# Optimization experiments

Measured on AMD Instinct MI355X. Metric: run time of the kernel, lower is better.

## Reference

```python
import jax, jax.numpy as jnp
import numpy as np
import math


def setup_inputs() -> dict:
    key = jax.random.key(0)
    k1, k2, k3 = jax.random.split(key, 3)
    b, h, s, d = 2, 16, 2048, 64
    q = jax.random.normal(k1, (b, h, s, d), dtype=jnp.float32)
    k = jax.random.normal(k2, (b, h, d, s), dtype=jnp.float32)  # pre-transposed as in the torch module
    v = jax.random.normal(k3, (b, h, s, d), dtype=jnp.float32)
    return {"q": q, "k": k, "v": v}


def reference(q, k, v):
    d = q.shape[-1]
    # unnormalized exp-attention, no max subtraction (faithful to source)
    p = jnp.exp(jnp.einsum('bhsd,bhdt->bhst', q, k) / math.sqrt(d))  # [b,h,s,s]
    attn = jnp.einsum('bhst,bhtd->bhsd', p, v)                        # [b,h,s,d]
    l = jnp.sum(p, axis=3, keepdims=True)                             # [b,h,s,1]
    return attn / l
```

## Files before the change

kernel.cpp:

```cpp
#include <hip/hip_runtime.h>

#define S_LEN 2048
#define D_DIM 64
#define BH 32
#define NN ((size_t)BH * S_LEN * D_DIM)

typedef short bf16x8 __attribute__((ext_vector_type(8)));
typedef float f32x16 __attribute__((ext_vector_type(16)));
typedef unsigned int u32x4 __attribute__((ext_vector_type(4)));

static __device__ __forceinline__ unsigned short f2bf(float x) {
  unsigned int u = __float_as_uint(x);
  u += 0x7fffu + ((u >> 16) & 1u);
  return (unsigned short)(u >> 16);
}
static __device__ __forceinline__ float bf2f(unsigned short h) {
  return __uint_as_float(((unsigned int)h) << 16);
}
static __device__ __forceinline__ void gll16(const void* g, void* l) {
  __builtin_amdgcn_global_load_lds((const __attribute__((address_space(1))) void*)g,
                                   (__attribute__((address_space(3))) void*)l, 16, 0, 0);
}

template <bool PERM, bool LO>
__global__ void transpose_split(const float* __restrict__ in,
                                unsigned short* __restrict__ outh,
                                unsigned short* __restrict__ outl,
                                int R, int C) {
  __shared__ float tile[64][65];
  const int bh = blockIdx.y;
  const int tilesPerRow = C >> 6;
  const int tr = blockIdx.x / tilesPerRow;
  const int tc = blockIdx.x % tilesPerRow;
  const int tid = threadIdx.x;
  const float* src = in + (size_t)bh * R * C;
  {
    const int c4 = (tid & 15) * 4;
    const int r0 = tid >> 4;
#pragma unroll
    for (int rep = 0; rep < 4; ++rep) {
      int r = r0 + rep * 16;
      float4 x = *(const float4*)&src[(size_t)(tr * 64 + r) * C + tc * 64 + c4];
      tile[r][c4] = x.x; tile[r][c4 + 1] = x.y; tile[r][c4 + 2] = x.z; tile[r][c4 + 3] = x.w;
    }
  }
  __syncthreads();
  unsigned short* oh = outh + (size_t)bh * R * C;
  unsigned short* ol = outl + (size_t)bh * R * C;
#pragma unroll
  for (int rep = 0; rep < 2; ++rep) {
    int ci = rep * 256 + tid;
    int orow = ci >> 3;
    int oslot = ci & 7;
    alignas(16) unsigned short hbuf[8];
    alignas(16) unsigned short lbuf[8];
#pragma unroll
    for (int i = 0; i < 8; ++i) {
      int p = oslot * 8 + i;
      int ridx = PERM ? ((p & ~15) | (p & 3) | ((p & 4) << 1) | ((p & 8) >> 1)) : p;
      float x = tile[ridx][orow];
      unsigned short hb = f2bf(x);
      hbuf[i] = hb;
      if (LO) lbuf[i] = f2bf(x - bf2f(hb));
    }
    size_t o = (size_t)(tc * 64 + orow) * R + tr * 64 + oslot * 8;
    *(int4*)&oh[o] = *(const int4*)hbuf;
    if (LO) *(int4*)&ol[o] = *(const int4*)lbuf;
  }
}

__global__ __launch_bounds__(256, 2) void attn_fused(
    const float* __restrict__ q, const unsigned short* __restrict__ Khg,
    const unsigned short* __restrict__ Klg, const unsigned short* __restrict__ Vhg,
    float* __restrict__ out) {
  __shared__ __align__(16) unsigned short smem[2][3][64][64];
  __shared__ float Lrow[4][32];

  const int bid = blockIdx.x;
  const int swz = (bid & 7) * 64 + (bid >> 3);
  const int bh = swz >> 4;
  const int qt = swz & 15;
  const int tid = threadIdx.x;
  const int w = tid >> 6;
  const int lane = tid & 63;
  const int l31 = lane & 31;
  const int h = lane >> 5;
  const int q0 = qt * 128 + w * 32;

  bf16x8 qh[4], ql[4];
  {
    const float* qb = q + ((size_t)bh * S_LEN + q0 + l31) * D_DIM;
#pragma unroll
    for (int ks = 0; ks < 4; ++ks) {
      const float* p = qb + ks * 16 + h * 8;
      float4 x0 = *(const float4*)p;
      float4 x1 = *(const float4*)(p + 4);
      float xs[8] = {x0.x, x0.y, x0.z, x0.w, x1.x, x1.y, x1.z, x1.w};
      bf16x8 hh, ll;
#pragma unroll
      for (int j = 0; j < 8; ++j) {
        unsigned short hb = f2bf(xs[j]);
        hh[j] = (short)hb;
        ll[j] = (short)f2bf(xs[j] - bf2f(hb));
      }
      qh[ks] = hh; ql[ks] = ll;
    }
  }

  int rowA[2], gsA[2];
#pragma unroll
  for (int r = 0; r < 2; ++r) {
    int c = (r * 4 + w) * 64 + lane;
    rowA[r] = c >> 3;
    gsA[r] = (c & 7) ^ ((c >> 3) & 7);
  }
  const unsigned short* Kh_b = Khg + (size_t)bh * S_LEN * D_DIM;
  const unsigned short* Kl_b = Klg + (size_t)bh * S_LEN * D_DIM;
  const unsigned short* Vh_b = Vhg + (size_t)bh * D_DIM * S_LEN;

  auto stage = [&](int buf, int bt) {
#pragma unroll
    for (int r = 0; r < 2; ++r) {
      const int row = rowA[r], gs = gsA[r];
      unsigned short* lbase = &smem[buf][0][0][0] + (r * 4 + w) * 512;
      gll16(Kh_b + (size_t)(bt + row) * 64 + gs * 8, lbase);
      gll16(Kl_b + (size_t)(bt + row) * 64 + gs * 8, lbase + 4096);
      gll16(Vh_b + (size_t)row * S_LEN + bt + gs * 8, lbase + 8192);
    }
  };

  f32x16 o[2] = {};
  float lsum = 0.f;
  const int kx = l31 & 7;

  stage(0, 0);
  __syncthreads();

  int cur = 0;
  for (int kt = 0; kt < 32; ++kt) {
    if (kt < 31) stage(cur ^ 1, (kt + 1) * 64);

    bf16x8 pa[4];
#pragma unroll
    for (int kt2 = 0; kt2 < 2; ++kt2) {
      f32x16 acc = {};
      const int krow = kt2 * 32 + l31;
      __builtin_amdgcn_s_setprio(1);
#pragma unroll
      for (int ks = 0; ks < 4; ++ks) {
        const int sl = ((ks * 2 + h) ^ kx) * 8;
        bf16x8 kh = *(const bf16x8*)&smem[cur][0][krow][sl];
        bf16x8 kl = *(const bf16x8*)&smem[cur][1][krow][sl];
        acc = __builtin_amdgcn_mfma_f32_32x32x16_bf16(kh, qh[ks], acc, 0, 0, 0);
        acc = __builtin_amdgcn_mfma_f32_32x32x16_bf16(kh, ql[ks], acc, 0, 0, 0);
        acc = __builtin_amdgcn_mfma_f32_32x32x16_bf16(kl, qh[ks], acc, 0, 0, 0);
      }
      __builtin_amdgcn_s_setprio(0);
      float pr[16];
#pragma unroll
      for (int i = 0; i < 16; ++i) {
        pr[i] = exp2f(acc[i] * 0.18033688011112042f);
        lsum += pr[i];
      }
#pragma unroll
      for (int s2 = 0; s2 < 2; ++s2) {
        u32x4 wds;
#pragma unroll
        for (int p2 = 0; p2 < 4; ++p2) {
          unsigned int pk;
          asm("v_cvt_pk_bf16_f32 %0, %1, %2"
              : "=v"(pk)
              : "v"(pr[s2 * 8 + p2 * 2]), "v"(pr[s2 * 8 + p2 * 2 + 1]));
          wds[p2] = pk;
        }
        pa[kt2 * 2 + s2] = __builtin_bit_cast(bf16x8, wds);
      }
    }

    __builtin_amdgcn_s_setprio(1);
#pragma unroll
    for (int s = 0; s < 4; ++s) {
#pragma unroll
      for (int db = 0; db < 2; ++db) {
        const int vrow = db * 32 + l31;
        const int sl = ((s * 2 + h) ^ kx) * 8;
        bf16x8 vh = *(const bf16x8*)&smem[cur][2][vrow][sl];
        o[db] = __builtin_amdgcn_mfma_f32_32x32x16_bf16(pa[s], vh, o[db], 0, 0, 0);
      }
    }
    __builtin_amdgcn_s_setprio(0);

    __syncthreads();
    cur ^= 1;
  }

  float fl = lsum + __shfl_xor(lsum, 32);
  float inv = 1.0f / fl;
  Lrow[w][l31] = inv;
  __syncthreads();
  float linv[16];
#pragma unroll
  for (int r = 0; r < 16; ++r) linv[r] = Lrow[w][(r & 3) + 8 * (r >> 2) + 4 * h];
  float* ob = out + ((size_t)bh * S_LEN + q0) * D_DIM;
#pragma unroll
  for (int db = 0; db < 2; ++db)
#pragma unroll
    for (int r = 0; r < 16; ++r) {
      const int qr = (r & 3) + 8 * (r >> 2) + 4 * h;
      ob[(size_t)qr * D_DIM + db * 32 + l31] = o[db][r] * linv[r];
    }
}

extern "C" void kernel_launch(void* const* d_in, const int* in_sizes, int n_in,
                              void* d_out, int out_size, void* d_ws, size_t ws_size,
                              hipStream_t stream) {
  const float* q = (const float*)d_in[0];
  const float* k = (const float*)d_in[1];
  const float* v = (const float*)d_in[2];
  float* out = (float*)d_out;
  unsigned short* ws = (unsigned short*)d_ws;
  unsigned short* Kh = ws;
  unsigned short* Kl = ws + NN;
  unsigned short* Vh = ws + 2 * NN;
  transpose_split<false, true><<<dim3(32, BH), 256, 0, stream>>>(k, Kh, Kl, 64, 2048);
  transpose_split<true, false><<<dim3(32, BH), 256, 0, stream>>>(v, Vh, nullptr, 2048, 64);
  attn_fused<<<dim3(512), 256, 0, stream>>>(q, Kh, Kl, Vh, out);
}
```

Measured before the change: 171.6 us.

## Split key tiles across wave pairs and pre-pack K/V in MFMA fragment order

The attention kernel now runs 512 threads per block. Each pair of waves shares a 32-row query tile, and each wave handles half of every 64-key tile. Partial outputs and row sums are combined through shared memory at the end. The K and V pack kernels now write data already laid out in MFMA operand fragment order, so LDS reads become simple lane-contiguous loads with no swizzle, and staging needs fewer address computations. This raises wave-level parallelism and occupancy, at the cost of a final cross-wave reduction, more waves contending for LDS, and a tighter per-thread register budget.

Result: faster. 164.3 us (-4.2%).

```diff
diff --git a/kernel.cpp b/kernel.cpp
--- a/kernel.cpp
+++ b/kernel.cpp
@@ -3,7 +3,7 @@
 #define S_LEN 2048
 #define D_DIM 64
 #define BH 32
-#define NN ((size_t)BH * S_LEN * D_DIM)
+#define NN ((size_t)131072)
 
 typedef short bf16x8 __attribute__((ext_vector_type(8)));
 typedef float f32x16 __attribute__((ext_vector_type(16)));
@@ -22,59 +22,72 @@
                                    (__attribute__((address_space(3))) void*)l, 16, 0, 0);
 }
 
-template <bool PERM, bool LO>
-__global__ void transpose_split(const float* __restrict__ in,
-                                unsigned short* __restrict__ outh,
-                                unsigned short* __restrict__ outl,
-                                int R, int C) {
+__global__ void pack_k(const float* __restrict__ in, unsigned short* __restrict__ oh,
+                       unsigned short* __restrict__ ol) {
   __shared__ float tile[64][65];
-  const int bh = blockIdx.y;
-  const int tilesPerRow = C >> 6;
-  const int tr = blockIdx.x / tilesPerRow;
-  const int tc = blockIdx.x % tilesPerRow;
-  const int tid = threadIdx.x;
-  const float* src = in + (size_t)bh * R * C;
-  {
-    const int c4 = (tid & 15) * 4;
-    const int r0 = tid >> 4;
-#pragma unroll
-    for (int rep = 0; rep < 4; ++rep) {
-      int r = r0 + rep * 16;
-      float4 x = *(const float4*)&src[(size_t)(tr * 64 + r) * C + tc * 64 + c4];
-      tile[r][c4] = x.x; tile[r][c4 + 1] = x.y; tile[r][c4 + 2] = x.z; tile[r][c4 + 3] = x.w;
-    }
-  }
-  __syncthreads();
-  unsigned short* oh = outh + (size_t)bh * R * C;
-  unsigned short* ol = outl + (size_t)bh * R * C;
+  const int bh = blockIdx.y, tc = blockIdx.x, tid = threadIdx.x;
+  const float* src = in + (size_t)bh * 64 * 2048;
+  const int c4 = (tid & 15) * 4, r0 = tid >> 4;
+#pragma unroll
+  for (int rep = 0; rep < 4; ++rep) {
+    int r = r0 + rep * 16;
+    float4 x = *(const float4*)&src[(size_t)r * 2048 + tc * 64 + c4];
+    tile[r][c4] = x.x; tile[r][c4 + 1] = x.y; tile[r][c4 + 2] = x.z; tile[r][c4 + 3] = x.w;
+  }
+  __syncthreads();
+  oh += (size_t)bh * NN; ol += (size_t)bh * NN;
 #pragma unroll
   for (int rep = 0; rep < 2; ++rep) {
-    int ci = rep * 256 + tid;
-    int orow = ci >> 3;
-    int oslot = ci & 7;
+    int unit = rep * 256 + tid;
+    int u = unit >> 6, t = unit & 63;
     alignas(16) unsigned short hbuf[8];
     alignas(16) unsigned short lbuf[8];
 #pragma unroll
-    for (int i = 0; i < 8; ++i) {
-      int p = oslot * 8 + i;
-      int ridx = PERM ? ((p & ~15) | (p & 3) | ((p & 4) << 1) | ((p & 8) >> 1)) : p;
-      float x = tile[ridx][orow];
+    for (int j = 0; j < 8; ++j) {
+      float x = tile[u * 8 + j][t];
       unsigned short hb = f2bf(x);
-      hbuf[i] = hb;
-      if (LO) lbuf[i] = f2bf(x - bf2f(hb));
-    }
-    size_t o = (size_t)(tc * 64 + orow) * R + tr * 64 + oslot * 8;
+      hbuf[j] = hb;
+      lbuf[j] = f2bf(x - bf2f(hb));
+    }
+    size_t o = ((size_t)u * 2048 + tc * 64 + t) * 8;
     *(int4*)&oh[o] = *(const int4*)hbuf;
-    if (LO) *(int4*)&ol[o] = *(const int4*)lbuf;
-  }
-}
-
-__global__ __launch_bounds__(256, 2) void attn_fused(
+    *(int4*)&ol[o] = *(const int4*)lbuf;
+  }
+}
+
+__global__ void pack_v(const float* __restrict__ in, unsigned short* __restrict__ oh) {
+  __shared__ float tile[64][65];
+  const int bh = blockIdx.y, tr = blockIdx.x, tid = threadIdx.x;
+  const float* src = in + (size_t)bh * 2048 * 64;
+  const int c4 = (tid & 15) * 4, r0 = tid >> 4;
+#pragma unroll
+  for (int rep = 0; rep < 4; ++rep) {
+    int r = r0 + rep * 16;
+    float4 x = *(const float4*)&src[(size_t)(tr * 64 + r) * 64 + c4];
+    tile[r][c4] = x.x; tile[r][c4 + 1] = x.y; tile[r][c4 + 2] = x.z; tile[r][c4 + 3] = x.w;
+  }
+  __syncthreads();
+  oh += (size_t)bh * NN;
+#pragma unroll
+  for (int rep = 0; rep < 2; ++rep) {
+    int unit = rep * 256 + tid;
+    int u = unit >> 6, d = unit & 63;
+    alignas(16) unsigned short hbuf[8];
+#pragma unroll
+    for (int j = 0; j < 8; ++j) {
+      int t_loc = (u >> 1) * 16 + (u & 1) * 4 + (j & 3) + 8 * (j >> 2);
+      hbuf[j] = f2bf(tile[t_loc][d]);
+    }
+    size_t o = ((size_t)(tr * 8 + u) * 64 + d) * 8;
+    *(int4*)&oh[o] = *(const int4*)hbuf;
+  }
+}
+
+__global__ __launch_bounds__(512, 4) void attn_fused(
     const float* __restrict__ q, const unsigned short* __restrict__ Khg,
     const unsigned short* __restrict__ Klg, const unsigned short* __restrict__ Vhg,
     float* __restrict__ out) {
-  __shared__ __align__(16) unsigned short smem[2][3][64][64];
-  __shared__ float Lrow[4][32];
+  __shared__ __align__(16) unsigned short smem[2][12288];
 
   const int bid = blockIdx.x;
   const int swz = (bid & 7) * 64 + (bid >> 3);
@@ -85,11 +98,12 @@
   const int lane = tid & 63;
   const int l31 = lane & 31;
   const int h = lane >> 5;
-  const int q0 = qt * 128 + w * 32;
+  const int qtile = w >> 1;
+  const int kh2 = w & 1;
 
   bf16x8 qh[4], ql[4];
   {
-    const float* qb = q + ((size_t)bh * S_LEN + q0 + l31) * D_DIM;
+    const float* qb = q + ((size_t)bh * S_LEN + qt * 128 + qtile * 32 + l31) * 64;
 #pragma unroll
     for (int ks = 0; ks < 4; ++ks) {
       const float* p = qb + ks * 16 + h * 8;
@@ -107,108 +121,115 @@
     }
   }
 
-  int rowA[2], gsA[2];
-#pragma unroll
-  for (int r = 0; r < 2; ++r) {
-    int c = (r * 4 + w) * 64 + lane;
-    rowA[r] = c >> 3;
-    gsA[r] = (c & 7) ^ ((c >> 3) & 7);
-  }
-  const unsigned short* Kh_b = Khg + (size_t)bh * S_LEN * D_DIM;
-  const unsigned short* Kl_b = Klg + (size_t)bh * S_LEN * D_DIM;
-  const unsigned short* Vh_b = Vhg + (size_t)bh * D_DIM * S_LEN;
-
-  auto stage = [&](int buf, int bt) {
-#pragma unroll
-    for (int r = 0; r < 2; ++r) {
-      const int row = rowA[r], gs = gsA[r];
-      unsigned short* lbase = &smem[buf][0][0][0] + (r * 4 + w) * 512;
-      gll16(Kh_b + (size_t)(bt + row) * 64 + gs * 8, lbase);
-      gll16(Kl_b + (size_t)(bt + row) * 64 + gs * 8, lbase + 4096);
-      gll16(Vh_b + (size_t)row * S_LEN + bt + gs * 8, lbase + 8192);
-    }
+  const unsigned short* srcp[3];
+  int stp[3], ldso[3];
+#pragma unroll
+  for (int i = 0; i < 3; ++i) {
+    int g = w * 3 + i;
+    int c = g & 7, typ = g >> 3;
+    if (typ < 2) {
+      size_t off = ((size_t)((c >> 1) * 2 + h) * 2048 + (c & 1) * 32 + l31) * 8;
+      srcp[i] = (typ == 0 ? Khg : Klg) + (size_t)bh * NN + off;
+      stp[i] = 512;
+      ldso[i] = typ * 4096 + c * 512;
+    } else {
+      size_t off = ((size_t)((c >> 1) * 2 + h) * 64 + (c & 1) * 32 + l31) * 8;
+      srcp[i] = Vhg + (size_t)bh * NN + off;
+      stp[i] = 4096;
+      ldso[i] = 8192 + c * 512;
+    }
+  }
+  auto stage = [&](int buf, int tile) {
+#pragma unroll
+    for (int i = 0; i < 3; ++i)
+      gll16(srcp[i] + (size_t)tile * stp[i], &smem[buf][ldso[i]]);
   };
 
-  f32x16 o[2] = {};
+  f32x16 o2[2] = {};
   float lsum = 0.f;
-  const int kx = l31 & 7;
+  const char* lp = (const char*)&smem[0][0] + lane * 16;
 
   stage(0, 0);
   __syncthreads();
 
-  int cur = 0;
-  for (int kt = 0; kt < 32; ++kt) {
-    if (kt < 31) stage(cur ^ 1, (kt + 1) * 64);
-
-    bf16x8 pa[4];
-#pragma unroll
-    for (int kt2 = 0; kt2 < 2; ++kt2) {
-      f32x16 acc = {};
-      const int krow = kt2 * 32 + l31;
-      __builtin_amdgcn_s_setprio(1);
-#pragma unroll
-      for (int ks = 0; ks < 4; ++ks) {
-        const int sl = ((ks * 2 + h) ^ kx) * 8;
-        bf16x8 kh = *(const bf16x8*)&smem[cur][0][krow][sl];
-        bf16x8 kl = *(const bf16x8*)&smem[cur][1][krow][sl];
-        acc = __builtin_amdgcn_mfma_f32_32x32x16_bf16(kh, qh[ks], acc, 0, 0, 0);
-        acc = __builtin_amdgcn_mfma_f32_32x32x16_bf16(kh, ql[ks], acc, 0, 0, 0);
-        acc = __builtin_amdgcn_mfma_f32_32x32x16_bf16(kl, qh[ks], acc, 0, 0, 0);
+  auto body = [&](int kt, int buf) {
+    if (kt < 31) stage(buf ^ 1, kt + 1);
+    const char* B = lp + buf * 24576;
+    f32x16 acc = {};
+    __builtin_amdgcn_s_setprio(1);
+#pragma unroll
+    for (int ks = 0; ks < 4; ++ks) {
+      bf16x8 kh = *(const bf16x8*)(B + (ks * 2 + kh2) * 1024);
+      bf16x8 kl = *(const bf16x8*)(B + 8192 + (ks * 2 + kh2) * 1024);
+      acc = __builtin_amdgcn_mfma_f32_32x32x16_bf16(kh, qh[ks], acc, 0, 0, 0);
+      acc = __builtin_amdgcn_mfma_f32_32x32x16_bf16(kh, ql[ks], acc, 0, 0, 0);
+      acc = __builtin_amdgcn_mfma_f32_32x32x16_bf16(kl, qh[ks], acc, 0, 0, 0);
+    }
+    __builtin_amdgcn_s_setprio(0);
+    float pr[16];
+#pragma unroll
+    for (int i = 0; i < 16; ++i) {
+      pr[i] = exp2f(acc[i] * 0.18033688011112042f);
+      lsum += pr[i];
+    }
+    bf16x8 pa[2];
+#pragma unroll
+    for (int s2 = 0; s2 < 2; ++s2) {
+      u32x4 wds;
+#pragma unroll
+      for (int p2 = 0; p2 < 4; ++p2) {
+        unsigned int pk;
+        asm("v_cvt_pk_bf16_f32 %0, %1, %2"
+            : "=v"(pk)
+            : "v"(pr[s2 * 8 + p2 * 2]), "v"(pr[s2 * 8 + p2 * 2 + 1]));
+        wds[p2] = pk;
       }
-      __builtin_amdgcn_s_setprio(0);
-      float pr[16];
-#pragma unroll
-      for (int i = 0; i < 16; ++i) {
-        pr[i] = exp2f(acc[i] * 0.18033688011112042f);
-        lsum += pr[i];
-      }
-#pragma unroll
-      for (int s2 = 0; s2 < 2; ++s2) {
-        u32x4 wds;
-#pragma unroll
-        for (int p2 = 0; p2 < 4; ++p2) {
-          unsigned int pk;
-          asm("v_cvt_pk_bf16_f32 %0, %1, %2"
-              : "=v"(pk)
-              : "v"(pr[s2 * 8 + p2 * 2]), "v"(pr[s2 * 8 + p2 * 2 + 1]));
-          wds[p2] = pk;
-        }
-        pa[kt2 * 2 + s2] = __builtin_bit_cast(bf16x8, wds);
-      }
-    }
-
+      pa[s2] = __builtin_bit_cast(bf16x8, wds);
+    }
     __builtin_amdgcn_s_setprio(1);
 #pragma unroll
-    for (int s = 0; s < 4; ++s) {
-#pragma unroll
-      for (int db = 0; db < 2; ++db) {
-        const int vrow = db * 32 + l31;
-        const int sl = ((s * 2 + h) ^ kx) * 8;
-        bf16x8 vh = *(const bf16x8*)&smem[cur][2][vrow][sl];
-        o[db] = __builtin_amdgcn_mfma_f32_32x32x16_bf16(pa[s], vh, o[db], 0, 0, 0);
-      }
+    for (int db = 0; db < 2; ++db) {
+      bf16x8 v0 = *(const bf16x8*)(B + 16384 + ((kh2 * 2 + 0) * 2 + db) * 1024);
+      bf16x8 v1 = *(const bf16x8*)(B + 16384 + ((kh2 * 2 + 1) * 2 + db) * 1024);
+      o2[db] = __builtin_amdgcn_mfma_f32_32x32x16_bf16(pa[0], v0, o2[db], 0, 0, 0);
+      o2[db] = __builtin_amdgcn_mfma_f32_32x32x16_bf16(pa[1], v1, o2[db], 0, 0, 0);
     }
     __builtin_amdgcn_s_setprio(0);
-
     __syncthreads();
-    cur ^= 1;
-  }
-
-  float fl = lsum + __shfl_xor(lsum, 32);
-  float inv = 1.0f / fl;
-  Lrow[w][l31] = inv;
-  __syncthreads();
-  float linv[16];
-#pragma unroll
-  for (int r = 0; r < 16; ++r) linv[r] = Lrow[w][(r & 3) + 8 * (r >> 2) + 4 * h];
-  float* ob = out + ((size_t)bh * S_LEN + q0) * D_DIM;
-#pragma unroll
-  for (int db = 0; db < 2; ++db)
-#pragma unroll
-    for (int r = 0; r < 16; ++r) {
-      const int qr = (r & 3) + 8 * (r >> 2) + 4 * h;
-      ob[(size_t)qr * D_DIM + db * 32 + l31] = o[db][r] * linv[r];
-    }
+  };
+
+  for (int kt = 0; kt < 32; kt += 2) {
+    body(kt, 0);
+    body(kt + 1, 1);
+  }
+
+  float ls = lsum + __shfl_xor(lsum, 32);
+  float* sc = (float*)&smem[0][0];
+  if (kh2 == 1) {
+#pragma unroll
+    for (int db = 0; db < 2; ++db)
+#pragma unroll
+      for (int r = 0; r < 16; ++r)
+        sc[(qtile * 2 + db) * 1024 + (h * 16 + r) * 32 + l31] = o2[db][r];
+    sc[8192 + qtile * 32 + l31] = ls;
+  }
+  __syncthreads();
+  if (kh2 == 1) return;
+  float ltot = ls + sc[8192 + qtile * 32 + l31];
+  float inv = 1.0f / ltot;
+  sc[8320 + qtile * 32 + l31] = inv;
+  asm volatile("s_waitcnt lgkmcnt(0)" ::: "memory");
+  float* ob = out + ((size_t)bh * S_LEN + qt * 128 + qtile * 32) * 64;
+#pragma unroll
+  for (int r = 0; r < 16; ++r) {
+    const int qr = (r & 3) + 8 * (r >> 2) + 4 * h;
+    float iv = sc[8320 + qtile * 32 + qr];
+#pragma unroll
+    for (int db = 0; db < 2; ++db) {
+      float val = (o2[db][r] + sc[(qtile * 2 + db) * 1024 + (h * 16 + r) * 32 + l31]) * iv;
+      ob[(size_t)qr * 64 + db * 32 + l31] = val;
+    }
+  }
 }
 
 extern "C" void kernel_launch(void* const* d_in, const int* in_sizes, int n_in,
@@ -220,9 +241,9 @@
   float* out = (float*)d_out;
   unsigned short* ws = (unsigned short*)d_ws;
   unsigned short* Kh = ws;
-  unsigned short* Kl = ws + NN;
-  unsigned short* Vh = ws + 2 * NN;
-  transpose_split<false, true><<<dim3(32, BH), 256, 0, stream>>>(k, Kh, Kl, 64, 2048);
-  transpose_split<true, false><<<dim3(32, BH), 256, 0, stream>>>(v, Vh, nullptr, 2048, 64);
-  attn_fused<<<dim3(512), 256, 0, stream>>>(q, Kh, Kl, Vh, out);
-}
+  unsigned short* Kl = ws + BH * NN;
+  unsigned short* Vh = ws + 2 * BH * NN;
+  pack_k<<<dim3(32, BH), 256, 0, stream>>>(k, Kh, Kl);
+  pack_v<<<dim3(32, BH), 256, 0, stream>>>(v, Vh);
+  attn_fused<<<dim3(512), 512, 0, stream>>>(q, Kh, Kl, Vh, out);
+}
```
